# Optimization experiments

Hardware: AMD Instinct MI355X
Metric: run time of the kernel (lower is better)

The kernel has to match this reference:

```python
import jax, jax.numpy as jnp
import numpy as np

NUM_HEADS = 8
N_POINTS = 9
OFFSET_SCALE = 4.0


def bilinear_sample(fmap_flat, xy, H, W):
    """fmap_flat: (BH, H*W, C) row-major spatial; xy: (BH, S, 2) pixel coords (x, y).
    grid_sample(mode='bilinear', padding_mode='zeros', align_corners=True) equivalent.
    Returns (BH, S, C)."""
    x, y = xy[..., 0], xy[..., 1]
    x0 = jnp.floor(x); y0 = jnp.floor(y)
    x1 = x0 + 1.0;    y1 = y0 + 1.0
    wx1 = x - x0; wx0 = 1.0 - wx1
    wy1 = y - y0; wy0 = 1.0 - wy1

    def corner(xi, yi, wgt):
        valid = (xi >= 0) & (xi <= W - 1) & (yi >= 0) & (yi <= H - 1)
        xi_c = jnp.clip(xi, 0, W - 1).astype(jnp.int32)
        yi_c = jnp.clip(yi, 0, H - 1).astype(jnp.int32)
        idx = yi_c * W + xi_c                                   # (BH, S)
        vals = jnp.take_along_axis(fmap_flat, idx[..., None], axis=1)  # (BH, S, C)
        return vals * (wgt * valid.astype(fmap_flat.dtype))[..., None]

    return (corner(x0, y0, wx0 * wy0) + corner(x1, y0, wx1 * wy0)
            + corner(x0, y1, wx0 * wy1) + corner(x1, y1, wx1 * wy1))


def setup_inputs() -> dict:
    key = jax.random.key(0)
    ks = jax.random.split(key, 10)
    B, N, D = 4, 6400, 256
    Hh, P = NUM_HEADS, N_POINTS
    s = 0.02
    return {
        "x":    jax.random.normal(ks[0], (B, N, D), dtype=jnp.float32),
        "Wq":   jax.random.normal(ks[1], (D, D), dtype=jnp.float32) * s,
        "bq":   jnp.zeros((D,), jnp.float32),
        "Woff": jax.random.normal(ks[2], (Hh * P * 2, D), dtype=jnp.float32) * s,
        "boff": jax.random.normal(ks[3], (Hh * P * 2,), dtype=jnp.float32) * s,
        "Wkv":  jax.random.normal(ks[4], (2 * D, D), dtype=jnp.float32) * s,
        "bkv":  jnp.zeros((2 * D,), jnp.float32),
        "Wout": jax.random.normal(ks[5], (D, D), dtype=jnp.float32) * s,
        "bout": jnp.zeros((D,), jnp.float32),
        "h": 40,
        "w": 160,
    }


def reference(x, Wq, bq, Woff, boff, Wkv, bkv, Wout, bout, h, w):
    B, N, D = x.shape
    H, P = NUM_HEADS, N_POINTS
    hd = D // H

    # queries: (B, H, N, hd)
    q = (x @ Wq.T + bq).reshape(B, N, H, hd).transpose(0, 2, 1, 3)

    # per-query per-head offsets in pixels: (B, N, H, P, 2) (dx, dy)
    offsets = jnp.tanh(x @ Woff.T + boff).reshape(B, N, H, P, 2) * OFFSET_SCALE

    # K/V feature maps via 1x1 conv == per-token linear; split heads, flat spatial
    kv = x @ Wkv.T + bkv                     # (B, N, 2D)
    k = kv[..., :D]
    v = kv[..., D:]
    k_flat = k.reshape(B, N, H, hd).transpose(0, 2, 1, 3).reshape(B * H, N, hd)
    v_flat = v.reshape(B, N, H, hd).transpose(0, 2, 1, 3).reshape(B * H, N, hd)

    # base pixel grid (x, y), row-major over (h, w)
    ys, xs = jnp.meshgrid(jnp.arange(h, dtype=x.dtype), jnp.arange(w, dtype=x.dtype), indexing="ij")
    base_xy = jnp.stack([xs, ys], axis=-1).reshape(N, 2)

    # sampling locations: (B, N, H, P, 2) -> (B*H, N*P, 2)
    sample_xy = base_xy[None, :, None, None, :] + offsets
    sample_xy = sample_xy.transpose(0, 2, 1, 3, 4).reshape(B * H, N * P, 2)

    sampled_k = bilinear_sample(k_flat, sample_xy, h, w).reshape(B, H, N, P, hd)
    sampled_v = bilinear_sample(v_flat, sample_xy, h, w).reshape(B, H, N, P, hd)

    logits = jnp.einsum("bhnd,bhnpd->bhnp", q, sampled_k) * (hd ** -0.5)
    attn = jax.nn.softmax(logits, axis=-1)
    out = jnp.einsum("bhnp,bhnpd->bhnd", attn, sampled_v)   # (B, H, N, hd)
    out = out.transpose(0, 2, 1, 3).reshape(B, N, D)
    return out @ Wout.T + bout
```

## Files before the change

### kernel.cpp

```cpp
#include <hip/hip_runtime.h>
#include <math.h>

#define BSZ    4
#define NTOK   6400
#define DMODEL 256
#define NHEAD  8
#define HDIM   32
#define NPTS   9
#define HSP    40
#define WSP    160
#define KDIM   256
#define MTOT   (BSZ*NTOK)

typedef short  short8  __attribute__((ext_vector_type(8)));
typedef float  floatx4 __attribute__((ext_vector_type(4)));
typedef float  f32x2   __attribute__((ext_vector_type(2)));

__device__ __forceinline__ ushort f2bf(float f) {
    uint u = __float_as_uint(f);
    u = (u + 0x7FFFu + ((u >> 16) & 1u)) >> 16;
    return (ushort)u;
}

__device__ __forceinline__ void unpack8v(uint4 u, f32x2* f) {
    f[0].x = __uint_as_float(u.x << 16); f[0].y = __uint_as_float(u.x & 0xFFFF0000u);
    f[1].x = __uint_as_float(u.y << 16); f[1].y = __uint_as_float(u.y & 0xFFFF0000u);
    f[2].x = __uint_as_float(u.z << 16); f[2].y = __uint_as_float(u.z & 0xFFFF0000u);
    f[3].x = __uint_as_float(u.w << 16); f[3].y = __uint_as_float(u.w & 0xFFFF0000u);
}

__device__ __forceinline__ float dot8(uint4 u, const f32x2* q2) {
    f32x2 a; a.x = 0.f; a.y = 0.f;
    f32x2 t;
    t.x = __uint_as_float(u.x << 16); t.y = __uint_as_float(u.x & 0xFFFF0000u);
    a += t * q2[0];
    t.x = __uint_as_float(u.y << 16); t.y = __uint_as_float(u.y & 0xFFFF0000u);
    a += t * q2[1];
    t.x = __uint_as_float(u.z << 16); t.y = __uint_as_float(u.z & 0xFFFF0000u);
    a += t * q2[2];
    t.x = __uint_as_float(u.w << 16); t.y = __uint_as_float(u.w & 0xFFFF0000u);
    a += t * q2[3];
    return a.x + a.y;
}

#define AS1C(p) ((const __attribute__((address_space(1))) void*)(p))
#define AS3(p)  ((__attribute__((address_space(3))) void*)(p))

__global__ __launch_bounds__(256) void cast_all(
    const float* __restrict__ x,   const float* __restrict__ Wq,
    const float* __restrict__ Woff,const float* __restrict__ Wkv,
    const float* __restrict__ Wout,
    ushort* __restrict__ xb, ushort* __restrict__ wf, ushort* __restrict__ woutb)
{
    const int bid = blockIdx.x;
    const int o = (bid < 1600) ? ((bid >> 3) + (bid & 7) * 200) : bid;
    if (o >= 1625 && o < 1632) {
        const int i = (o - 1625) * 4096 + threadIdx.x * 4;
        ushort4 z; z.x = 0; z.y = 0; z.z = 0; z.w = 0;
        #pragma unroll
        for (int k = 0; k < 4; ++k)
            *(ushort4*)(wf + 400 * 256 + i + k * 1024) = z;
        return;
    }
    const float* src; ushort* dst; int base;
    if      (o < 1600) { src = x;    dst = xb;              base = o; }
    else if (o < 1616) { src = Wq;   dst = wf;              base = o - 1600; }
    else if (o < 1625) { src = Woff; dst = wf + 256 * 256;  base = o - 1616; }
    else if (o < 1664) { src = Wkv;  dst = wf + 512 * 256;  base = o - 1632; }
    else               { src = Wout; dst = woutb;           base = o - 1664; }
    const int i0 = base * 4096 + threadIdx.x * 4;
    float4 v[4];
    #pragma unroll
    for (int k = 0; k < 4; ++k) v[k] = *(const float4*)(src + i0 + k * 1024);
    #pragma unroll
    for (int k = 0; k < 4; ++k) {
        ushort4 o4;
        o4.x = f2bf(v[k].x); o4.y = f2bf(v[k].y);
        o4.z = f2bf(v[k].z); o4.w = f2bf(v[k].w);
        *(ushort4*)(dst + i0 + k * 1024) = o4;
    }
}

template <int MODE>
__global__ __launch_bounds__(256) void gemm64(
    const ushort* __restrict__ Xb,
    const ushort* __restrict__ Wf,
    const float* __restrict__ bq, const float* __restrict__ boff,
    const float* __restrict__ bkv,
    ushort* __restrict__ qb, short* __restrict__ offp,
    ushort* __restrict__ kfb, ushort* __restrict__ vfb,
    float* __restrict__ Yout)
{
    constexpr int NBN = (MODE == 0) ? 16 : 4;
    __shared__ ushort As[2][64 * 64];
    __shared__ ushort Bs[2][64 * 64];

    const int tid = threadIdx.x;
    const int bid = blockIdx.x;
    const int xcd = bid & 7;
    const int j   = bid >> 3;
    const int block_n = (j % NBN) * 64;
    const int block_m = (xcd * 50 + j / NBN) * 64;

    const int wave = tid >> 6, lane = tid & 63;
    const int wr = (wave >> 1) * 32, wc = (wave & 1) * 32;
    const int l15 = lane & 15, quad = lane >> 4;

    const int srow  = lane >> 3;
    const int sslot = (lane & 7) ^ srow;

    floatx4 acc[2][2];
    #pragma unroll
    for (int i = 0; i < 2; ++i)
        #pragma unroll
        for (int jj = 0; jj < 2; ++jj) {
            acc[i][jj][0] = 0.f; acc[i][jj][1] = 0.f;
            acc[i][jj][2] = 0.f; acc[i][jj][3] = 0.f;
        }

    auto stage = [&](int buf, int kt) {
        #pragma unroll
        for (int i = 0; i < 2; ++i) {
            const int rb = wave * 16 + i * 8;
            const ushort* sa = Xb + (size_t)(block_m + rb + srow) * KDIM + kt + sslot * 8;
            const ushort* sb = Wf + (size_t)(block_n + rb + srow) * KDIM + kt + sslot * 8;
            __builtin_amdgcn_global_load_lds(AS1C(sa), AS3(&As[buf][rb * 64]), 16, 0, 0);
            __builtin_amdgcn_global_load_lds(AS1C(sb), AS3(&Bs[buf][rb * 64]), 16, 0, 0);
        }
    };

    auto compute = [&](int buf) {
        #pragma unroll
        for (int ks2 = 0; ks2 < 2; ++ks2) {
            short8 af[2], bfr[2];
            #pragma unroll
            for (int f = 0; f < 2; ++f) {
                const int ra  = wr + f * 16 + l15;
                const int rbb = wc + f * 16 + l15;
                const int sl  = (((ks2 * 4 + quad) ^ (l15 & 7))) * 8;
                af[f]  = *(const short8*)&As[buf][ra * 64 + sl];
                bfr[f] = *(const short8*)&Bs[buf][rbb * 64 + sl];
            }
            #pragma unroll
            for (int fm = 0; fm < 2; ++fm)
                #pragma unroll
                for (int fn = 0; fn < 2; ++fn)
                    acc[fm][fn] = __builtin_amdgcn_mfma_f32_16x16x32_bf16(
                        af[fm], bfr[fn], acc[fm][fn], 0, 0, 0);
        }
    };

    stage(0, 0);
    __syncthreads();
    #pragma unroll
    for (int t = 0; t < 3; ++t) {
        stage((t + 1) & 1, (t + 1) * 64);
        compute(t & 1);
        __syncthreads();
    }
    compute(1);

    const int bb  = block_m / NTOK;
    const int nn0 = block_m - bb * NTOK;
    #pragma unroll
    for (int fn = 0; fn < 2; ++fn) {
        const int col = block_n + wc + fn * 16 + l15;
        float bcol;
        if (MODE == 1) {
            bcol = bq[col];
        } else {
            if      (col < 256) bcol = bq[col];
            else if (col < 400) bcol = boff[col - 256];
            else if (col < 512) bcol = 0.f;
            else                bcol = bkv[col - 512];
        }
        #pragma unroll
        for (int fm = 0; fm < 2; ++fm) {
            #pragma unroll
            for (int r = 0; r < 4; ++r) {
                const int rloc = wr + fm * 16 + quad * 4 + r;
                const int row  = block_m + rloc;
                const float val = acc[fm][fn][r] + bcol;
                if (MODE == 1) {
                    Yout[(size_t)row * DMODEL + col] = val;
                } else {
                    if (col < 256) {
                        qb[(size_t)row * DMODEL + col] = f2bf(val);
                    } else if (col < 400) {
                        offp[(size_t)row * 144 + (col - 256)] =
                            (short)__float2int_rn(tanhf(val) * 16384.0f);
                    } else if (col >= 512) {
                        const int c2 = col - 512;
                        const int hh = (c2 & 255) >> 5, cc = c2 & 31;
                        const int nn = nn0 + rloc;
                        const size_t o = (((size_t)(bb * NHEAD + hh)) * NTOK + nn) * HDIM + cc;
                        if (c2 < 256) kfb[o] = f2bf(val);
                        else          vfb[o] = f2bf(val);
                    }
                }
            }
        }
    }
}

__global__ __launch_bounds__(256, 3) void deform_attn(
    const ushort* __restrict__ qb,
    const short* __restrict__ offp,
    const ushort* __restrict__ kfb,
    const ushort* __restrict__ vfb,
    ushort* __restrict__ attnb)
{
    const int lane = threadIdx.x & 63;
    const int o = ((int)blockIdx.x >> 3) + ((int)blockIdx.x & 7) * 400;
    const int token = o * 8 + (threadIdx.x >> 6) * 2 + (lane >> 5);
    const int h = (lane >> 2) & 7, lc = lane & 3;
    const int b = token / NTOK, n = token % NTOK;

    const uint4 qu = *(const uint4*)(qb + (size_t)token * DMODEL + h * HDIM + lc * 8);
    f32x2 q2[4]; unpack8v(qu, q2);
    #pragma unroll
    for (int i = 0; i < 4; ++i) q2[i] *= 0.17677669529663687f;

    const short* ob = offp + (size_t)token * 144 + h * (NPTS * 2);
    const float bx = (float)(n % WSP), by = (float)(n / WSP);
    const ushort* kbase = kfb + (size_t)(b * NHEAD + h) * NTOK * HDIM + lc * 8;
    const ushort* vbase = vfb + (size_t)(b * NHEAD + h) * NTOK * HDIM + lc * 8;

    const bool interior = (bx >= 4.0f) & (bx <= 154.0f) & (by >= 4.0f) & (by <= 34.0f);
    int   idxO[3][4];
    float wtO[3][4];
    #pragma unroll
    for (int i = 0; i < 3; ++i) {
        const int p = min(lc * 3 + i, NPTS - 1);
        const int u = *(const int*)(ob + 2 * p);
        const float ofx = (float)((short)(u & 0xFFFF)) * (1.0f / 4096.0f);
        const float ofy = (float)(u >> 16) * (1.0f / 4096.0f);
        const float sx = bx + ofx, sy = by + ofy;
        const float fx0 = floorf(sx), fy0 = floorf(sy);
        const float wx1 = sx - fx0, wx0 = 1.0f - wx1;
        const float wy1 = sy - fy0, wy0 = 1.0f - wy1;
        if (interior) {
            const int i00 = ((int)fy0 * WSP + (int)fx0) * HDIM;
            wtO[i][0] = wx0 * wy0; wtO[i][1] = wx1 * wy0;
            wtO[i][2] = wx0 * wy1; wtO[i][3] = wx1 * wy1;
            idxO[i][0] = i00;
            idxO[i][1] = i00 + HDIM;
            idxO[i][2] = i00 + WSP * HDIM;
            idxO[i][3] = i00 + WSP * HDIM + HDIM;
        } else {
            const int ix0 = (int)fx0, iy0 = (int)fy0;
            const int ix1 = ix0 + 1, iy1 = iy0 + 1;
            const bool vx0 = (ix0 >= 0) & (ix0 <= WSP - 1);
            const bool vx1 = (ix1 >= 0) & (ix1 <= WSP - 1);
            const bool vy0 = (iy0 >= 0) & (iy0 <= HSP - 1);
            const bool vy1 = (iy1 >= 0) & (iy1 <= HSP - 1);
            const int cx0 = min(max(ix0, 0), WSP - 1);
            const int cx1 = min(max(ix1, 0), WSP - 1);
            const int cy0 = min(max(iy0, 0), HSP - 1);
            const int cy1 = min(max(iy1, 0), HSP - 1);
            wtO[i][0] = wx0 * wy0 * (float)(vx0 && vy0);
            wtO[i][1] = wx1 * wy0 * (float)(vx1 && vy0);
            wtO[i][2] = wx0 * wy1 * (float)(vx0 && vy1);
            wtO[i][3] = wx1 * wy1 * (float)(vx1 && vy1);
            idxO[i][0] = (cy0 * WSP + cx0) * HDIM;
            idxO[i][1] = (cy0 * WSP + cx1) * HDIM;
            idxO[i][2] = (cy1 * WSP + cx0) * HDIM;
            idxO[i][3] = (cy1 * WSP + cx1) * HDIM;
        }
    }

    float s = 0.f;
    f32x2 o2[4];
    #pragma unroll
    for (int i = 0; i < 4; ++i) { o2[i].x = 0.f; o2[i].y = 0.f; }

    #pragma unroll
    for (int g = 0; g < 3; ++g) {
        const int src = (lane & 60) | g;
        int   idx[3][4];
        float wt[3][4];
        #pragma unroll
        for (int jj = 0; jj < 3; ++jj) {
            #pragma unroll
            for (int c = 0; c < 4; ++c) {
                idx[jj][c] = __shfl(idxO[jj][c], src, 64);
                wt[jj][c]  = __shfl(wtO[jj][c], src, 64);
            }
        }

        uint4 ku[12], vu[12];
        #pragma unroll
        for (int jj = 0; jj < 3; ++jj)
            #pragma unroll
            for (int c = 0; c < 4; ++c)
                ku[jj * 4 + c] = *(const uint4*)(kbase + idx[jj][c]);
        #pragma unroll
        for (int jj = 0; jj < 3; ++jj)
            #pragma unroll
            for (int c = 0; c < 4; ++c)
                vu[jj * 4 + c] = *(const uint4*)(vbase + idx[jj][c]);

        float l[3];
        #pragma unroll
        for (int jj = 0; jj < 3; ++jj) {
            float part = wt[jj][0] * dot8(ku[jj * 4 + 0], q2)
                       + wt[jj][1] * dot8(ku[jj * 4 + 1], q2)
                       + wt[jj][2] * dot8(ku[jj * 4 + 2], q2)
                       + wt[jj][3] * dot8(ku[jj * 4 + 3], q2);
            part += __shfl_xor(part, 1, 64);
            part += __shfl_xor(part, 2, 64);
            l[jj] = part;
        }

        const float e0 = __expf(l[0]);
        const float e1 = __expf(l[1]);
        const float e2 = __expf(l[2]);
        s += e0 + e1 + e2;
        const float e[3] = {e0, e1, e2};

        #pragma unroll
        for (int jj = 0; jj < 3; ++jj) {
            #pragma unroll
            for (int c = 0; c < 4; ++c) {
                f32x2 vv[4]; unpack8v(vu[jj * 4 + c], vv);
                const float ew = e[jj] * wt[jj][c];
                #pragma unroll
                for (int i = 0; i < 4; ++i) o2[i] += vv[i] * ew;
            }
        }
    }

    const float inv = 1.0f / s;
    uint4 ru;
    ru.x = (uint)f2bf(o2[0].x * inv) | ((uint)f2bf(o2[0].y * inv) << 16);
    ru.y = (uint)f2bf(o2[1].x * inv) | ((uint)f2bf(o2[1].y * inv) << 16);
    ru.z = (uint)f2bf(o2[2].x * inv) | ((uint)f2bf(o2[2].y * inv) << 16);
    ru.w = (uint)f2bf(o2[3].x * inv) | ((uint)f2bf(o2[3].y * inv) << 16);
    *(uint4*)(attnb + (size_t)token * DMODEL + h * HDIM + lc * 8) = ru;
}

extern "C" void kernel_launch(void* const* d_in, const int* in_sizes, int n_in,
                              void* d_out, int out_size, void* d_ws, size_t ws_size,
                              hipStream_t stream) {
    const float* x    = (const float*)d_in[0];
    const float* Wq   = (const float*)d_in[1];
    const float* bq   = (const float*)d_in[2];
    const float* Woff = (const float*)d_in[3];
    const float* boff = (const float*)d_in[4];
    const float* Wkv  = (const float*)d_in[5];
    const float* bkv  = (const float*)d_in[6];
    const float* Wout = (const float*)d_in[7];
    const float* bout = (const float*)d_in[8];

    ushort* xb    = (ushort*)d_ws;
    ushort* qb    = xb + (size_t)MTOT * DMODEL;
    short*  offp  = (short*)(qb + (size_t)MTOT * DMODEL);
    ushort* kfb   = (ushort*)(offp + (size_t)MTOT * 144);
    ushort* vfb   = kfb + (size_t)MTOT * DMODEL;
    ushort* wf    = vfb + (size_t)MTOT * DMODEL;
    ushort* woutb = wf + 262144;
    ushort* attnb = xb;

    cast_all<<<dim3(1680), dim3(256), 0, stream>>>(x, Wq, Woff, Wkv, Wout,
                                                   xb, wf, woutb);

    gemm64<0><<<dim3(6400), dim3(256), 0, stream>>>(xb, wf, bq, boff, bkv,
                                                    qb, offp, kfb, vfb, nullptr);

    deform_attn<<<dim3(3200), dim3(256), 0, stream>>>(qb, offp, kfb, vfb, attnb);

    gemm64<1><<<dim3(1600), dim3(256), 0, stream>>>(attnb, woutb, bout,
                                                    nullptr, nullptr, nullptr,
                                                    nullptr, nullptr, nullptr,
                                                    (float*)d_out);
}
```

Before: 188.2 us.

## Skip dead padding column tile and stage GEMM epilogue through LDS for vector stores

The fused projection GEMM previously launched 16 column tiles per row block, including one tile (columns 448-511) that only covers padding and writes nothing. Its grid shrinks to 15 column tiles, remapping indices to skip that tile. The q/k/v epilogue tiles now write bf16 results into swizzled shared memory and then emit 16-byte vectorized global stores, replacing scattered 2-byte stores. This adds a barrier and LDS traffic in the epilogue to get coalesced writes.

```diff
diff --git a/kernel.cpp b/kernel.cpp
--- a/kernel.cpp
+++ b/kernel.cpp
@@ -91,16 +91,22 @@
     ushort* __restrict__ kfb, ushort* __restrict__ vfb,
     float* __restrict__ Yout)
 {
-    constexpr int NBN = (MODE == 0) ? 16 : 4;
-    __shared__ ushort As[2][64 * 64];
-    __shared__ ushort Bs[2][64 * 64];
+    __shared__ __align__(16) ushort As[2][64 * 64];
+    __shared__ __align__(16) ushort Bs[2][64 * 64];
 
     const int tid = threadIdx.x;
     const int bid = blockIdx.x;
     const int xcd = bid & 7;
     const int j   = bid >> 3;
-    const int block_n = (j % NBN) * 64;
-    const int block_m = (xcd * 50 + j / NBN) * 64;
+    int block_n, block_m;
+    if (MODE == 0) {
+        int jn = j % 15; if (jn >= 7) ++jn;
+        block_n = jn * 64;
+        block_m = (xcd * 50 + j / 15) * 64;
+    } else {
+        block_n = (j % 4) * 64;
+        block_m = (xcd * 50 + j / 4) * 64;
+    }
 
     const int wave = tid >> 6, lane = tid & 63;
     const int wr = (wave >> 1) * 32, wc = (wave & 1) * 32;
@@ -162,40 +168,67 @@
 
     const int bb  = block_m / NTOK;
     const int nn0 = block_m - bb * NTOK;
-    #pragma unroll
-    for (int fn = 0; fn < 2; ++fn) {
-        const int col = block_n + wc + fn * 16 + l15;
-        float bcol;
-        if (MODE == 1) {
-            bcol = bq[col];
-        } else {
-            if      (col < 256) bcol = bq[col];
-            else if (col < 400) bcol = boff[col - 256];
-            else if (col < 512) bcol = 0.f;
-            else                bcol = bkv[col - 512];
-        }
-        #pragma unroll
-        for (int fm = 0; fm < 2; ++fm) {
-            #pragma unroll
-            for (int r = 0; r < 4; ++r) {
-                const int rloc = wr + fm * 16 + quad * 4 + r;
-                const int row  = block_m + rloc;
-                const float val = acc[fm][fn][r] + bcol;
-                if (MODE == 1) {
-                    Yout[(size_t)row * DMODEL + col] = val;
-                } else {
-                    if (col < 256) {
-                        qb[(size_t)row * DMODEL + col] = f2bf(val);
-                    } else if (col < 400) {
+
+    if (MODE == 0 && (block_n < 256 || block_n >= 512)) {
+        ushort* Cs = &As[0][0];
+        #pragma unroll
+        for (int fn = 0; fn < 2; ++fn) {
+            const int col = block_n + wc + fn * 16 + l15;
+            const float bcol = (block_n < 256) ? bq[col] : bkv[col - 512];
+            #pragma unroll
+            for (int fm = 0; fm < 2; ++fm) {
+                #pragma unroll
+                for (int r = 0; r < 4; ++r) {
+                    const int lrow  = wr + fm * 16 + quad * 4 + r;
+                    const int lcol  = wc + fn * 16 + l15;
+                    const int lcolS = lcol ^ (((lrow >> 2) & 3) << 4);
+                    Cs[lrow * 64 + lcolS] = f2bf(acc[fm][fn][r] + bcol);
+                }
+            }
+        }
+        __syncthreads();
+        #pragma unroll
+        for (int p = 0; p < 2; ++p) {
+            const int s    = p * 256 + tid;
+            const int lrow = s >> 3;
+            const int seg8 = s & 7;
+            const int q4   = (lrow >> 2) & 3;
+            const int c0p  = (seg8 & 1) * 8 + (((seg8 >> 1) ^ q4) << 4);
+            const uint4 v = *(const uint4*)&Cs[lrow * 64 + c0p];
+            if (block_n < 256) {
+                *(uint4*)&qb[(size_t)(block_m + lrow) * DMODEL + block_n + seg8 * 8] = v;
+            } else {
+                const int c2 = block_n - 512 + seg8 * 8;
+                const int hh = (c2 & 255) >> 5, cc = c2 & 31;
+                const int nn = nn0 + lrow;
+                const size_t dsto = (((size_t)(bb * NHEAD + hh)) * NTOK + nn) * HDIM + cc;
+                if (c2 < 256) *(uint4*)&kfb[dsto] = v;
+                else          *(uint4*)&vfb[dsto] = v;
+            }
+        }
+    } else {
+        #pragma unroll
+        for (int fn = 0; fn < 2; ++fn) {
+            const int col = block_n + wc + fn * 16 + l15;
+            float bcol;
+            if (MODE == 1) {
+                bcol = bq[col];
+            } else {
+                if      (col < 400) bcol = boff[col - 256];
+                else                bcol = 0.f;
+            }
+            #pragma unroll
+            for (int fm = 0; fm < 2; ++fm) {
+                #pragma unroll
+                for (int r = 0; r < 4; ++r) {
+                    const int rloc = wr + fm * 16 + quad * 4 + r;
+                    const int row  = block_m + rloc;
+                    const float val = acc[fm][fn][r] + bcol;
+                    if (MODE == 1) {
+                        Yout[(size_t)row * DMODEL + col] = val;
+                    } else if (col >= 256 && col < 400) {
                         offp[(size_t)row * 144 + (col - 256)] =
                             (short)__float2int_rn(tanhf(val) * 16384.0f);
-                    } else if (col >= 512) {
-                        const int c2 = col - 512;
-                        const int hh = (c2 & 255) >> 5, cc = c2 & 31;
-                        const int nn = nn0 + rloc;
-                        const size_t o = (((size_t)(bb * NHEAD + hh)) * NTOK + nn) * HDIM + cc;
-                        if (c2 < 256) kfb[o] = f2bf(val);
-                        else          vfb[o] = f2bf(val);
                     }
                 }
             }
@@ -364,7 +397,7 @@
     cast_all<<<dim3(1680), dim3(256), 0, stream>>>(x, Wq, Woff, Wkv, Wout,
                                                    xb, wf, woutb);
 
-    gemm64<0><<<dim3(6400), dim3(256), 0, stream>>>(xb, wf, bq, boff, bkv,
+    gemm64<0><<<dim3(6000), dim3(256), 0, stream>>>(xb, wf, bq, boff, bkv,
                                                     qb, offp, kfb, vfb, nullptr);
 
     deform_attn<<<dim3(3200), dim3(256), 0, stream>>>(qb, offp, kfb, vfb, attnb);
```

Result: faster. 179.6 us (-4.5%).
